# Kernel tuning notes

Measured on AMD Instinct MI355X. Metric: run time of the kernel, lower is better.

Reference implementation:

```python
import jax, jax.numpy as jnp
import numpy as np

N = 100_000   # nodes
E = 3_200_000 # edges
F = 13        # input features
H = 64        # hidden dim
G = 512       # graphs in batch
C = 2         # output classes
BN_EPS = 1e-5


def _linear(key, fan_in, fan_out):
    kw, kb = jax.random.split(key)
    bound = 1.0 / np.sqrt(fan_in)
    W = jax.random.uniform(kw, (fan_in, fan_out), jnp.float32, -bound, bound)
    b = jax.random.uniform(kb, (fan_out,), jnp.float32, -bound, bound)
    return W, b


def _conv_params(key, fin, fout):
    k1, k2, k3 = jax.random.split(key, 3)
    W1, b1 = _linear(k1, fin, fout)
    W2, b2 = _linear(k2, fout, fout)
    gamma = jnp.ones((fout,), jnp.float32)
    beta = jnp.zeros((fout,), jnp.float32)
    mean = jax.random.normal(k3, (fout,), jnp.float32) * 0.1
    var = jnp.ones((fout,), jnp.float32)
    return W1, b1, gamma, beta, mean, var, W2, b2


def setup_inputs() -> dict:
    key = jax.random.key(0)
    ks = jax.random.split(key, 10)
    x = jax.random.normal(ks[0], (N, F), jnp.float32)
    src = jax.random.randint(ks[1], (E,), 0, N, jnp.int32)
    dst = jax.random.randint(ks[2], (E,), 0, N, jnp.int32)
    batch = jnp.sort(jax.random.randint(ks[3], (N,), 0, G, jnp.int32))
    inp = {"x": x, "src": src, "dst": dst, "batch": batch}
    for i, name in enumerate(["c1", "c2", "c3"]):
        fin = F if i == 0 else H
        W1, b1, g, be, m, v, W2, b2 = _conv_params(ks[4 + i], fin, H)
        inp.update({f"{name}_W1": W1, f"{name}_b1": b1, f"{name}_g": g,
                    f"{name}_be": be, f"{name}_m": m, f"{name}_v": v,
                    f"{name}_W2": W2, f"{name}_b2": b2})
    inp["fc1_W"], inp["fc1_b"] = _linear(ks[7], 3 * H, 3 * H)
    inp["fc2_W"], inp["fc2_b"] = _linear(ks[8], 3 * H, C)
    return inp


def _mlp(h, W1, b1, g, be, m, v, W2, b2):
    # Linear -> BatchNorm1d (inference, running stats) -> ReLU -> Linear -> ReLU
    h = h @ W1 + b1
    h = (h - m) * jax.lax.rsqrt(v + BN_EPS) * g + be
    h = jax.nn.relu(h)
    return jax.nn.relu(h @ W2 + b2)


def _gin_conv(x, src, dst, mlp_params):
    # GINConv with eps=0: MLP(x + sum_{j->i} x_j) via scatter-add over edges
    agg = jax.ops.segment_sum(x[src], dst, num_segments=N)
    return _mlp(x + agg, *mlp_params)


def reference(x, src, dst, batch,
              c1_W1, c1_b1, c1_g, c1_be, c1_m, c1_v, c1_W2, c1_b2,
              c2_W1, c2_b1, c2_g, c2_be, c2_m, c2_v, c2_W2, c2_b2,
              c3_W1, c3_b1, c3_g, c3_be, c3_m, c3_v, c3_W2, c3_b2,
              fc1_W, fc1_b, fc2_W, fc2_b):
    h1 = jax.nn.relu(_gin_conv(x, src, dst, (c1_W1, c1_b1, c1_g, c1_be, c1_m, c1_v, c1_W2, c1_b2)))
    h2 = jax.nn.relu(_gin_conv(h1, src, dst, (c2_W1, c2_b1, c2_g, c2_be, c2_m, c2_v, c2_W2, c2_b2)))
    h3 = jax.nn.relu(_gin_conv(h2, src, dst, (c3_W1, c3_b1, c3_g, c3_be, c3_m, c3_v, c3_W2, c3_b2)))
    p1 = jax.ops.segment_sum(h1, batch, num_segments=G)
    p2 = jax.ops.segment_sum(h2, batch, num_segments=G)
    p3 = jax.ops.segment_sum(h3, batch, num_segments=G)
    h = jnp.concatenate([p1, p2, p3], axis=1)  # [G, 3H]
    h = jax.nn.relu(h @ fc1_W + fc1_b)
    # Dropout is identity in eval mode
    h = h @ fc2_W + fc2_b
    return jax.nn.log_softmax(h, axis=-1)
```

## Files before the change

kernel.cpp:

```cpp
#include <hip/hip_runtime.h>

#define NNODES 100000
#define NEDGES 3200000
#define NF 13
#define NFP 16
#define NG 512
#define BN_EPS 1e-5f
#define NTILES (NNODES / 16)

#define BSH 9
#define NBUCK ((NNODES + 511) / 512)
#define PTILE 4096
#define NPBLK ((NEDGES + PTILE - 1) / PTILE)
#define EPT (PTILE / 256)
#define SCAP 17664
#define CVTB 200
#define K1B (NPBLK + 12 + CVTB)

typedef __attribute__((ext_vector_type(8))) _Float16 f16x8;
typedef __attribute__((ext_vector_type(4))) _Float16 f16x4;
typedef __attribute__((ext_vector_type(4))) float f32x4;
typedef __attribute__((ext_vector_type(4))) int i32x4;

__device__ __forceinline__ unsigned short f2h(float f) {
    union { _Float16 h; unsigned short u; } c;
    c.h = (_Float16)f;
    return c.u;
}
__device__ __forceinline__ float h2f(unsigned short u) {
    union { _Float16 h; unsigned short u; } c;
    c.u = u;
    return (float)c.h;
}

__device__ __forceinline__ f16x8 shfl_xor8(f16x8 v, int m) {
    union { f16x8 h; int i[4]; } a, b;
    a.h = v;
#pragma unroll
    for (int k = 0; k < 4; ++k) b.i[k] = __shfl_xor(a.i[k], m, 64);
    return b.h;
}
__device__ __forceinline__ f16x4 shfl_xor4(f16x4 v, int m) {
    union { f16x4 h; int i[2]; } a, b;
    a.h = v;
#pragma unroll
    for (int k = 0; k < 2; ++k) b.i[k] = __shfl_xor(a.i[k], m, 64);
    return b.h;
}

__launch_bounds__(256)
__global__ void prep_sort_kernel(const int* __restrict__ src, const int* __restrict__ dst,
                                 int* __restrict__ pairout, int* __restrict__ bseg,
                                 const float* __restrict__ x, unsigned short* __restrict__ xh,
                                 const float* __restrict__ w10, const float* __restrict__ w20,
                                 const float* __restrict__ w11, const float* __restrict__ w21,
                                 const float* __restrict__ w12, const float* __restrict__ w22,
                                 unsigned short* __restrict__ wfrag) {
    __shared__ int hist[256];
    __shared__ int scanbuf[256];
    __shared__ int spair[PTILE];
    int t = threadIdx.x;
    int bid = blockIdx.x;

    if (bid < NPBLK) {
        int base = bid * PTILE;
        int cnt = NEDGES - base; if (cnt > PTILE) cnt = PTILE;
        int v[EPT], b[EPT];
#pragma unroll
        for (int j = 0; j < EPT; ++j) {
            int i = t + j * 256;
            if (i < cnt) {
                int d = __builtin_nontemporal_load(dst + base + i);
                int s = __builtin_nontemporal_load(src + base + i);
                b[j] = d >> BSH;
                v[j] = ((d & 511) << 17) | s;
            } else b[j] = -1;
        }
        hist[t] = 0;
        __syncthreads();
#pragma unroll
        for (int j = 0; j < EPT; ++j)
            if (b[j] >= 0) atomicAdd(&hist[b[j]], 1);
        __syncthreads();
        int val = hist[t];
        scanbuf[t] = val;
        __syncthreads();
        for (int off = 1; off < 256; off <<= 1) {
            int add = (t >= off) ? scanbuf[t - off] : 0;
            __syncthreads();
            scanbuf[t] += add;
            __syncthreads();
        }
        int excl = scanbuf[t] - val;
        if (t < NBUCK) bseg[(size_t)bid * NBUCK + t] = (excl << 13) | val;
        hist[t] = excl;
        __syncthreads();
#pragma unroll
        for (int j = 0; j < EPT; ++j) {
            if (b[j] >= 0) {
                int pos = atomicAdd(&hist[b[j]], 1);
                spair[pos] = v[j];
            }
        }
        __syncthreads();
        const i32x4* sp4 = (const i32x4*)spair;
        i32x4* po4 = (i32x4*)(pairout + (size_t)bid * PTILE);
        for (int j = t; j < PTILE / 4; j += 256)
            __builtin_nontemporal_store(sp4[j], po4 + j);
    } else if (bid < NPBLK + 12) {
        int tid = (bid - NPBLK) * 256 + t;
        if (tid >= 3072) return;
        int layer = tid >> 10;
        int rem = tid & 1023;
        int mat = rem >> 9;
        int tile = (rem >> 7) & 3;
        int chunk = (rem >> 6) & 1;
        int lane = rem & 63;
        int quad = lane >> 4, n = lane & 15;
        const float* W = (layer == 0) ? (mat ? w20 : w10)
                       : (layer == 1) ? (mat ? w21 : w11)
                                      : (mat ? w22 : w12);
        int K = (layer == 0 && mat == 0) ? NF : 64;
        unsigned short* o = wfrag + ((size_t)tid) * 8;
#pragma unroll
        for (int j = 0; j < 8; ++j) {
            int k = chunk * 32 + quad * 8 + j;
            float val = (k < K) ? W[k * 64 + tile * 16 + n] : 0.f;
            o[j] = f2h(val);
        }
    } else {
        const int total = NNODES * NFP;
        int idx = (bid - NPBLK - 12) * 256 + t;
        int stride = CVTB * 256;
        for (int i = idx; i < total; i += stride) {
            int n = i >> 4;
            int f = i & 15;
            xh[i] = (f < NF) ? f2h(__builtin_nontemporal_load(x + n * NF + f))
                             : (unsigned short)0;
        }
    }
}

__launch_bounds__(1024)
__global__ void bucket_sort_kernel(const int* __restrict__ pairout,
                                   const int* __restrict__ bseg,
                                   int2* __restrict__ rowse,
                                   int* __restrict__ csre) {
    __shared__ int scanbuf[1024];
    __shared__ int soff[NPBLK];
    __shared__ int hcur[512];
    __shared__ int shv[1];
    __shared__ int spair[SCAP];
    __shared__ int ssort[SCAP];
    int bk = blockIdx.x;
    int t = threadIdx.x;
    int lo = bk << BSH;
    int wave = t >> 6, lane = t & 63;
    int bbase = bk * SCAP;

    int c = (t < NPBLK) ? (bseg[(size_t)t * NBUCK + bk] & 8191) : 0;
    scanbuf[t] = c;
    __syncthreads();
    for (int off = 1; off < 1024; off <<= 1) {
        int a = (t >= off) ? scanbuf[t - off] : 0;
        __syncthreads();
        scanbuf[t] += a;
        __syncthreads();
    }
    if (t < NPBLK) soff[t] = scanbuf[t] - c;
    if (t == NPBLK - 1) shv[0] = scanbuf[t];
    __syncthreads();
    int total = shv[0]; if (total > SCAP) total = SCAP;

    for (int k = wave; k < NPBLK; k += 16) {
        int pk = bseg[(size_t)k * NBUCK + bk];
        int cnt = pk & 8191;
        const int* seg = pairout + (size_t)k * PTILE + (pk >> 13);
        int dsto = soff[k];
        for (int i = lane; i < cnt; i += 64)
            if (dsto + i < SCAP) spair[dsto + i] = __builtin_nontemporal_load(seg + i);
    }
    if (t < 512) hcur[t] = 0;
    __syncthreads();

    for (int i = t; i < total; i += 1024) atomicAdd(&hcur[spair[i] >> 17], 1);
    __syncthreads();

    int hv = (t < 512) ? hcur[t] : 0;
    scanbuf[t] = hv;
    __syncthreads();
    for (int off = 1; off < 1024; off <<= 1) {
        int a = (t >= off) ? scanbuf[t - off] : 0;
        __syncthreads();
        scanbuf[t] += a;
        __syncthreads();
    }
    if (t < 512) {
        int excl = scanbuf[t] - hv;
        hcur[t] = excl;
        if (lo + t < NNODES) {
            int2 se; se.x = bbase + excl; se.y = bbase + excl + hv;
            rowse[lo + t] = se;
        }
    }
    __syncthreads();

    for (int i = t; i < total; i += 1024) {
        int p = spair[i];
        int pos = atomicAdd(&hcur[p >> 17], 1);
        ssort[pos] = p & 0x1FFFF;
    }
    __syncthreads();

    for (int i = t; i < total; i += 1024)
        __builtin_nontemporal_store(ssort[i], csre + bbase + i);
}

template <int LAYER>
__launch_bounds__(256, 4)
__global__ void gin_layer_kernel(const unsigned short* __restrict__ xin,
                                 const int2* __restrict__ rowse,
                                 const int* __restrict__ csr,
                                 const unsigned short* __restrict__ wfrag,
                                 const float* __restrict__ b1, const float* __restrict__ gam,
                                 const float* __restrict__ be, const float* __restrict__ mu,
                                 const float* __restrict__ var, const float* __restrict__ b2,
                                 unsigned short* __restrict__ hout) {
    constexpr int FSTR = (LAYER == 1) ? NFP : 64;
    __shared__ __align__(16) unsigned short ytile[16][80];
    __shared__ __align__(16) unsigned short ztile[16][80];
    int lane = threadIdx.x & 63;
    int wid = threadIdx.x >> 6;
    int quad = lane >> 4, n16 = lane & 15;
    int nb = blockIdx.x * 16;

    if constexpr (LAYER == 1) {
        int g = lane >> 2;
        int r = lane & 3;
#pragma unroll
        for (int pp = 0; pp < 2; ++pp) {
            int lnA = wid * 4 + pp * 2;
            int nA = nb + lnA, nB = nA + 1;
            int2 seA = rowse[nA];
            int2 seB = rowse[nB];
            int jA = seA.x, endA = seA.y;
            int jB = seB.x, endB = seB.y;
            f16x4 accA = {0, 0, 0, 0};
            f16x4 accB = {0, 0, 0, 0};
            if (g == 0) {
                accA = *(const f16x4*)&xin[(size_t)nA * FSTR + r * 4];
                accB = *(const f16x4*)&xin[(size_t)nB * FSTR + r * 4];
            }
            while (jA + 16 <= endA && jB + 16 <= endB) {
                int iA = __builtin_nontemporal_load(csr + jA + g);
                int iB = __builtin_nontemporal_load(csr + jB + g);
                f16x4 vA = *(const f16x4*)&xin[(size_t)iA * FSTR + r * 4];
                f16x4 vB = *(const f16x4*)&xin[(size_t)iB * FSTR + r * 4];
                accA += vA; accB += vB;
                jA += 16; jB += 16;
            }
            for (; jA + 32 <= endA; jA += 32) {
                int i0 = __builtin_nontemporal_load(csr + jA + g);
                int i1 = __builtin_nontemporal_load(csr + jA + 16 + g);
                f16x4 v0 = *(const f16x4*)&xin[(size_t)i0 * FSTR + r * 4];
                f16x4 v1 = *(const f16x4*)&xin[(size_t)i1 * FSTR + r * 4];
                accA += v0; accA += v1;
            }
            for (; jA < endA; jA += 16) {
                int e = jA + g;
                if (e < endA) {
                    int i0 = __builtin_nontemporal_load(csr + e);
                    accA += *(const f16x4*)&xin[(size_t)i0 * FSTR + r * 4];
                }
            }
            for (; jB + 32 <= endB; jB += 32) {
                int i0 = __builtin_nontemporal_load(csr + jB + g);
                int i1 = __builtin_nontemporal_load(csr + jB + 16 + g);
                f16x4 v0 = *(const f16x4*)&xin[(size_t)i0 * FSTR + r * 4];
                f16x4 v1 = *(const f16x4*)&xin[(size_t)i1 * FSTR + r * 4];
                accB += v0; accB += v1;
            }
            for (; jB < endB; jB += 16) {
                int e = jB + g;
                if (e < endB) {
                    int i0 = __builtin_nontemporal_load(csr + e);
                    accB += *(const f16x4*)&xin[(size_t)i0 * FSTR + r * 4];
                }
            }
#pragma unroll
            for (int m = 4; m < 64; m <<= 1) {
                accA += shfl_xor4(accA, m);
                accB += shfl_xor4(accB, m);
            }
            if (g == 0) {
                *(f16x4*)&ytile[lnA][r * 4] = accA;
                *(f16x4*)&ytile[lnA + 1][r * 4] = accB;
            } else if (g == 1) {
                f16x4 z = {0, 0, 0, 0};
                *(f16x4*)&ytile[lnA][16 + r * 4] = z;
                *(f16x4*)&ytile[lnA + 1][16 + r * 4] = z;
            }
        }
    } else {
        int g = lane >> 3;
        int r = lane & 7;
#pragma unroll
        for (int pp = 0; pp < 2; ++pp) {
            int lnA = wid * 4 + pp * 2;
            int nA = nb + lnA, nB = nA + 1;
            int2 seA = rowse[nA];
            int2 seB = rowse[nB];
            int jA = seA.x, endA = seA.y;
            int jB = seB.x, endB = seB.y;
            f16x8 accA = {0, 0, 0, 0, 0, 0, 0, 0};
            f16x8 accB = {0, 0, 0, 0, 0, 0, 0, 0};
            if (g == 0) {
                accA = *(const f16x8*)&xin[(size_t)nA * 64 + r * 8];
                accB = *(const f16x8*)&xin[(size_t)nB * 64 + r * 8];
            }
            while (jA + 16 <= endA && jB + 16 <= endB) {
                int iA0 = __builtin_nontemporal_load(csr + jA + g);
                int iA1 = __builtin_nontemporal_load(csr + jA + 8 + g);
                int iB0 = __builtin_nontemporal_load(csr + jB + g);
                int iB1 = __builtin_nontemporal_load(csr + jB + 8 + g);
                f16x8 vA0 = *(const f16x8*)&xin[(size_t)iA0 * 64 + r * 8];
                f16x8 vA1 = *(const f16x8*)&xin[(size_t)iA1 * 64 + r * 8];
                f16x8 vB0 = *(const f16x8*)&xin[(size_t)iB0 * 64 + r * 8];
                f16x8 vB1 = *(const f16x8*)&xin[(size_t)iB1 * 64 + r * 8];
                accA += vA0; accA += vA1;
                accB += vB0; accB += vB1;
                jA += 16; jB += 16;
            }
            for (; jA + 16 <= endA; jA += 16) {
                int i0 = __builtin_nontemporal_load(csr + jA + g);
                int i1 = __builtin_nontemporal_load(csr + jA + 8 + g);
                f16x8 v0 = *(const f16x8*)&xin[(size_t)i0 * 64 + r * 8];
                f16x8 v1 = *(const f16x8*)&xin[(size_t)i1 * 64 + r * 8];
                accA += v0; accA += v1;
            }
            for (; jA < endA; jA += 8) {
                int e = jA + g;
                if (e < endA) {
                    int i0 = __builtin_nontemporal_load(csr + e);
                    accA += *(const f16x8*)&xin[(size_t)i0 * 64 + r * 8];
                }
            }
            for (; jB + 16 <= endB; jB += 16) {
                int i0 = __builtin_nontemporal_load(csr + jB + g);
                int i1 = __builtin_nontemporal_load(csr + jB + 8 + g);
                f16x8 v0 = *(const f16x8*)&xin[(size_t)i0 * 64 + r * 8];
                f16x8 v1 = *(const f16x8*)&xin[(size_t)i1 * 64 + r * 8];
                accB += v0; accB += v1;
            }
            for (; jB < endB; jB += 8) {
                int e = jB + g;
                if (e < endB) {
                    int i0 = __builtin_nontemporal_load(csr + e);
                    accB += *(const f16x8*)&xin[(size_t)i0 * 64 + r * 8];
                }
            }
#pragma unroll
            for (int m = 8; m < 64; m <<= 1) {
                accA += shfl_xor8(accA, m);
                accB += shfl_xor8(accB, m);
            }
            if (g == 0) {
                *(f16x8*)&ytile[lnA][r * 8] = accA;
                *(f16x8*)&ytile[lnA + 1][r * 8] = accB;
            }
        }
    }

    const f16x8* wf = (const f16x8*)wfrag;
    f16x8 w1f0 = wf[((0 * 4 + wid) * 2 + 0) * 64 + lane];
    f16x8 w1f1 = (LAYER == 2) ? wf[((0 * 4 + wid) * 2 + 1) * 64 + lane] : w1f0;
    f16x8 w2f0 = wf[((1 * 4 + wid) * 2 + 0) * 64 + lane];
    f16x8 w2f1 = wf[((1 * 4 + wid) * 2 + 1) * 64 + lane];
    int f = wid * 16 + n16;
    float sc = gam[f] * rsqrtf(var[f] + BN_EPS);
    float sh = (b1[f] - mu[f]) * sc + be[f];
    float bb2 = b2[f];

    __syncthreads();

    f16x8 a0 = *(const f16x8*)&ytile[n16][quad * 8];
    f32x4 z4 = {0.f, 0.f, 0.f, 0.f};
    z4 = __builtin_amdgcn_mfma_f32_16x16x32_f16(a0, w1f0, z4, 0, 0, 0);
    if constexpr (LAYER == 2) {
        f16x8 a1 = *(const f16x8*)&ytile[n16][32 + quad * 8];
        z4 = __builtin_amdgcn_mfma_f32_16x16x32_f16(a1, w1f1, z4, 0, 0, 0);
    }
#pragma unroll
    for (int reg = 0; reg < 4; ++reg) {
        float z = fmaxf(fmaf(z4[reg], sc, sh), 0.f);
        ztile[quad * 4 + reg][wid * 16 + n16] = f2h(z);
    }
    __syncthreads();

    f16x8 az0 = *(const f16x8*)&ztile[n16][quad * 8];
    f16x8 az1 = *(const f16x8*)&ztile[n16][32 + quad * 8];
    f32x4 h4 = {0.f, 0.f, 0.f, 0.f};
    h4 = __builtin_amdgcn_mfma_f32_16x16x32_f16(az0, w2f0, h4, 0, 0, 0);
    h4 = __builtin_amdgcn_mfma_f32_16x16x32_f16(az1, w2f1, h4, 0, 0, 0);
#pragma unroll
    for (int reg = 0; reg < 4; ++reg) {
        float h = fmaxf(h4[reg] + bb2, 0.f);
        hout[(size_t)(nb + quad * 4 + reg) * 64 + wid * 16 + n16] = f2h(h);
    }
}

__launch_bounds__(192)
__global__ void poolhead_kernel(const unsigned short* __restrict__ h1,
                                const unsigned short* __restrict__ h2,
                                const unsigned short* __restrict__ h3,
                                const int* __restrict__ batch,
                                const float* __restrict__ fc1W, const float* __restrict__ fc1b,
                                const float* __restrict__ fc2W, const float* __restrict__ fc2b,
                                float* __restrict__ out) {
    __shared__ float ps[192];
    __shared__ float hs[192];
    int gi = blockIdx.x;
    int t = threadIdx.x;

    int l = 0, r = NNODES;
    while (l < r) { int m = (l + r) >> 1; if (batch[m] < gi) l = m + 1; else r = m; }
    int lo = l;
    r = NNODES;
    while (l < r) { int m = (l + r) >> 1; if (batch[m] < gi + 1) l = m + 1; else r = m; }
    int hi = l;

    int layer = t >> 6, lane = t & 63;
    const unsigned short* hb = (layer == 0) ? h1 : (layer == 1) ? h2 : h3;
    float acc = 0.f;
    for (int n = lo; n < hi; ++n)
        acc += h2f(__builtin_nontemporal_load(hb + (size_t)n * 64 + lane));
    ps[t] = acc;
    __syncthreads();

    float a = fc1b[t];
#pragma unroll 8
    for (int k = 0; k < 192; ++k) a = fmaf(ps[k], fc1W[k * 192 + t], a);
    hs[t] = fmaxf(a, 0.f);
    __syncthreads();
    if (t == 0) {
        float l0 = fc2b[0], l1 = fc2b[1];
        for (int k = 0; k < 192; ++k) {
            float h = hs[k];
            l0 = fmaf(h, fc2W[k * 2 + 0], l0);
            l1 = fmaf(h, fc2W[k * 2 + 1], l1);
        }
        float mx = fmaxf(l0, l1);
        float lse = mx + logf(expf(l0 - mx) + expf(l1 - mx));
        out[gi * 2 + 0] = l0 - lse;
        out[gi * 2 + 1] = l1 - lse;
    }
}

extern "C" void kernel_launch(void* const* d_in, const int* in_sizes, int n_in,
                              void* d_out, int out_size, void* d_ws, size_t ws_size,
                              hipStream_t stream) {
    const float* x = (const float*)d_in[0];
    const int* src = (const int*)d_in[1];
    const int* dst = (const int*)d_in[2];
    const int* batch = (const int*)d_in[3];
    const float* c1[8];
    const float* c2[8];
    const float* c3[8];
    for (int i = 0; i < 8; ++i) {
        c1[i] = (const float*)d_in[4 + i];
        c2[i] = (const float*)d_in[12 + i];
        c3[i] = (const float*)d_in[20 + i];
    }
    const float* fc1W = (const float*)d_in[28];
    const float* fc1b = (const float*)d_in[29];
    const float* fc2W = (const float*)d_in[30];
    const float* fc2b = (const float*)d_in[31];
    float* out = (float*)d_out;

    unsigned short* base = (unsigned short*)d_ws;
    const size_t NA = (size_t)NNODES * 64;
    unsigned short* xh  = base;
    unsigned short* h1  = xh + (size_t)NNODES * NFP;
    unsigned short* h2  = h1 + NA;
    unsigned short* h3  = h2 + NA;
    unsigned short* wfrag = h3 + NA;
    int* ibase = (int*)(wfrag + 3 * 8192);
    int2* rowse  = (int2*)ibase;
    int* csre    = ibase + 2 * NNODES;
    int* pairout = csre + (size_t)NBUCK * SCAP + 256;
    int* bseg    = pairout + (size_t)NPBLK * PTILE;

    prep_sort_kernel<<<K1B, 256, 0, stream>>>(
        src, dst, pairout, bseg, x, xh,
        c1[0], c1[6], c2[0], c2[6], c3[0], c3[6], wfrag);

    bucket_sort_kernel<<<NBUCK, 1024, 0, stream>>>(pairout, bseg, rowse, csre);

    gin_layer_kernel<1><<<NTILES, 256, 0, stream>>>(
        xh, rowse, csre, wfrag + 0 * 8192,
        c1[1], c1[2], c1[3], c1[4], c1[5], c1[7], h1);
    gin_layer_kernel<2><<<NTILES, 256, 0, stream>>>(
        h1, rowse, csre, wfrag + 1 * 8192,
        c2[1], c2[2], c2[3], c2[4], c2[5], c2[7], h2);
    gin_layer_kernel<2><<<NTILES, 256, 0, stream>>>(
        h2, rowse, csre, wfrag + 2 * 8192,
        c3[1], c3[2], c3[3], c3[4], c3[5], c3[7], h3);

    poolhead_kernel<<<NG, 192, 0, stream>>>(
        h1, h2, h3, batch, fc1W, fc1b, fc2W, fc2b, out);
}
```

Measured before the change: 443.9 us.

## Split pooling into chunked atomic pool kernel and separate head kernel

Global pooling moves out of the per-graph head kernel, which used one 192-thread block per graph walking roughly 195 nodes serially. The new pool kernel gives each wave a 64-node chunk of one layer and flushes partial sums with atomicAdd whenever the graph id changes. The pool buffer is zeroed by extra blocks in the prep kernel. This trades more parallelism in the pooling reads for an added kernel launch, float atomics and nondeterministic summation order.

```diff
diff --git a/kernel.cpp b/kernel.cpp
--- a/kernel.cpp
+++ b/kernel.cpp
@@ -15,7 +15,11 @@
 #define EPT (PTILE / 256)
 #define SCAP 17664
 #define CVTB 200
-#define K1B (NPBLK + 12 + CVTB)
+#define PZB 8
+#define K1B (NPBLK + 12 + CVTB + PZB)
+
+#define NCHUNK ((NNODES + 63) / 64)
+#define NPTASK (3 * NCHUNK)
 
 typedef __attribute__((ext_vector_type(8))) _Float16 f16x8;
 typedef __attribute__((ext_vector_type(4))) _Float16 f16x4;
@@ -55,7 +59,8 @@
                                  const float* __restrict__ w10, const float* __restrict__ w20,
                                  const float* __restrict__ w11, const float* __restrict__ w21,
                                  const float* __restrict__ w12, const float* __restrict__ w22,
-                                 unsigned short* __restrict__ wfrag) {
+                                 unsigned short* __restrict__ wfrag,
+                                 float* __restrict__ pool) {
     __shared__ int hist[256];
     __shared__ int scanbuf[256];
     __shared__ int spair[PTILE];
@@ -128,7 +133,7 @@
             float val = (k < K) ? W[k * 64 + tile * 16 + n] : 0.f;
             o[j] = f2h(val);
         }
-    } else {
+    } else if (bid < NPBLK + 12 + CVTB) {
         const int total = NNODES * NFP;
         int idx = (bid - NPBLK - 12) * 256 + t;
         int stride = CVTB * 256;
@@ -138,6 +143,13 @@
             xh[i] = (f < NF) ? f2h(__builtin_nontemporal_load(x + n * NF + f))
                              : (unsigned short)0;
         }
+    } else {
+        const int total4 = NG * 192 / 4;
+        int idx = (bid - NPBLK - 12 - CVTB) * 256 + t;
+        int stride = PZB * 256;
+        f32x4 z = {0.f, 0.f, 0.f, 0.f};
+        f32x4* p4 = (f32x4*)pool;
+        for (int i = idx; i < total4; i += stride) p4[i] = z;
     }
 }
 
@@ -409,38 +421,48 @@
     }
 }
 
-__launch_bounds__(192)
-__global__ void poolhead_kernel(const unsigned short* __restrict__ h1,
-                                const unsigned short* __restrict__ h2,
-                                const unsigned short* __restrict__ h3,
-                                const int* __restrict__ batch,
-                                const float* __restrict__ fc1W, const float* __restrict__ fc1b,
-                                const float* __restrict__ fc2W, const float* __restrict__ fc2b,
-                                float* __restrict__ out) {
+__launch_bounds__(256)
+__global__ void pool_kernel(const unsigned short* __restrict__ h1,
+                            const unsigned short* __restrict__ h2,
+                            const unsigned short* __restrict__ h3,
+                            const int* __restrict__ batch,
+                            float* __restrict__ pool) {
+    int task = blockIdx.x * 4 + (threadIdx.x >> 6);
+    if (task >= NPTASK) return;
+    int lane = threadIdx.x & 63;
+    int layer = task / NCHUNK;
+    int c = task - layer * NCHUNK;
+    int n0 = c * 64;
+    int n1 = n0 + 64; if (n1 > NNODES) n1 = NNODES;
+    const unsigned short* hb = (layer == 0) ? h1 : (layer == 1) ? h2 : h3;
+    float acc = 0.f;
+    int curg = batch[n0];
+    for (int n = n0; n < n1; ++n) {
+        int gid = batch[n];
+        if (gid != curg) {
+            atomicAdd(&pool[(size_t)curg * 192 + layer * 64 + lane], acc);
+            acc = 0.f;
+            curg = gid;
+        }
+        acc += h2f(__builtin_nontemporal_load(hb + (size_t)n * 64 + lane));
+    }
+    atomicAdd(&pool[(size_t)curg * 192 + layer * 64 + lane], acc);
+}
+
+__global__ void head_kernel(const float* __restrict__ pool,
+                            const float* __restrict__ fc1W, const float* __restrict__ fc1b,
+                            const float* __restrict__ fc2W, const float* __restrict__ fc2b,
+                            float* __restrict__ out) {
     __shared__ float ps[192];
     __shared__ float hs[192];
     int gi = blockIdx.x;
     int t = threadIdx.x;
-
-    int l = 0, r = NNODES;
-    while (l < r) { int m = (l + r) >> 1; if (batch[m] < gi) l = m + 1; else r = m; }
-    int lo = l;
-    r = NNODES;
-    while (l < r) { int m = (l + r) >> 1; if (batch[m] < gi + 1) l = m + 1; else r = m; }
-    int hi = l;
-
-    int layer = t >> 6, lane = t & 63;
-    const unsigned short* hb = (layer == 0) ? h1 : (layer == 1) ? h2 : h3;
-    float acc = 0.f;
-    for (int n = lo; n < hi; ++n)
-        acc += h2f(__builtin_nontemporal_load(hb + (size_t)n * 64 + lane));
-    ps[t] = acc;
-    __syncthreads();
-
-    float a = fc1b[t];
+    ps[t] = pool[gi * 192 + t];
+    __syncthreads();
+    float acc = fc1b[t];
 #pragma unroll 8
-    for (int k = 0; k < 192; ++k) a = fmaf(ps[k], fc1W[k * 192 + t], a);
-    hs[t] = fmaxf(a, 0.f);
+    for (int k = 0; k < 192; ++k) acc = fmaf(ps[k], fc1W[k * 192 + t], acc);
+    hs[t] = fmaxf(acc, 0.f);
     __syncthreads();
     if (t == 0) {
         float l0 = fc2b[0], l1 = fc2b[1];
@@ -484,7 +506,8 @@
     unsigned short* h2  = h1 + NA;
     unsigned short* h3  = h2 + NA;
     unsigned short* wfrag = h3 + NA;
-    int* ibase = (int*)(wfrag + 3 * 8192);
+    float* pool = (float*)(wfrag + 3 * 8192);
+    int* ibase = (int*)(pool + (size_t)NG * 192);
     int2* rowse  = (int2*)ibase;
     int* csre    = ibase + 2 * NNODES;
     int* pairout = csre + (size_t)NBUCK * SCAP + 256;
@@ -492,7 +515,7 @@
 
     prep_sort_kernel<<<K1B, 256, 0, stream>>>(
         src, dst, pairout, bseg, x, xh,
-        c1[0], c1[6], c2[0], c2[6], c3[0], c3[6], wfrag);
+        c1[0], c1[6], c2[0], c2[6], c3[0], c3[6], wfrag, pool);
 
     bucket_sort_kernel<<<NBUCK, 1024, 0, stream>>>(pairout, bseg, rowse, csre);
 
@@ -506,6 +529,6 @@
         h2, rowse, csre, wfrag + 2 * 8192,
         c3[1], c3[2], c3[3], c3[4], c3[5], c3[7], h3);
 
-    poolhead_kernel<<<NG, 192, 0, stream>>>(
-        h1, h2, h3, batch, fc1W, fc1b, fc2W, fc2b, out);
-}
+    pool_kernel<<<(NPTASK + 3) / 4, 256, 0, stream>>>(h1, h2, h3, batch, pool);
+    head_kernel<<<NG, 192, 0, stream>>>(pool, fc1W, fc1b, fc2W, fc2b, out);
+}
```

Result: faster. 413.9 us (-6.8%).
